# Optimization experiments

Measured on AMD Instinct MI355X. Metric: run time of the kernel, lower is better.

The kernel has to match this reference:

```python
import jax, jax.numpy as jnp
import numpy as np

N_NODES = 100000


def _gcn_conv(x, W, b, src, dst, num_nodes):
    """PyG GCNConv: h = x @ W; symmetric-normalized scatter-add over edges
    (self-loops already included in src/dst); out = aggregate + b."""
    h = x @ W  # [N, out]
    ones = jnp.ones(src.shape[0], dtype=x.dtype)
    deg = jax.ops.segment_sum(ones, dst, num_segments=num_nodes)  # in-degree incl self-loop
    dinv = jnp.where(deg > 0, jax.lax.rsqrt(deg), 0.0)
    norm = dinv[src] * dinv[dst]  # [E]
    msg = h[src] * norm[:, None]  # [E, out] -- dominant memory traffic
    out = jax.ops.segment_sum(msg, dst, num_segments=num_nodes)
    return out + b


def setup_inputs() -> dict:
    key = jax.random.key(0)
    k = jax.random.split(key, 4)
    in_c, hid, out_c = 128, 64, 32
    n_edges = 1600000
    x = jax.random.normal(k[0], (N_NODES, in_c), dtype=jnp.float32)
    edge_index = jax.random.randint(k[1], (2, n_edges), 0, N_NODES, dtype=jnp.int64)
    W1 = jax.random.normal(k[2], (in_c, hid), dtype=jnp.float32) * (1.0 / np.sqrt(in_c))
    b1 = jnp.zeros((hid,), dtype=jnp.float32)
    W2 = jax.random.normal(k[3], (hid, out_c), dtype=jnp.float32) * (1.0 / np.sqrt(hid))
    b2 = jnp.zeros((out_c,), dtype=jnp.float32)
    return {"x": x, "edge_index": edge_index, "W1": W1, "b1": b1, "W2": W2, "b2": b2}


def reference(x, edge_index, W1, b1, W2, b2):
    num_nodes = x.shape[0]
    loops = jnp.arange(num_nodes, dtype=edge_index.dtype)
    src = jnp.concatenate([edge_index[0], loops])  # add self-loops once, shared by both layers
    dst = jnp.concatenate([edge_index[1], loops])
    h = _gcn_conv(x, W1, b1, src, dst, num_nodes)
    h = jax.nn.relu(h)
    out = _gcn_conv(h, W2, b2, src, dst, num_nodes)
    return out
```

## Files before the change

kernel.cpp:

```cpp
#include <hip/hip_runtime.h>


#define NBKT(n) (((n) + 127) >> 7)

__device__ inline float bf2f(unsigned short u) {
    union { unsigned int i; float f; } v;
    v.i = ((unsigned int)u) << 16;
    return v.f;
}
__device__ inline unsigned short f2bf(float f) {
    union { float f; unsigned int i; } v;
    v.f = f;
    unsigned int u = v.i;
    return (unsigned short)((u + 0x7fff + ((u >> 16) & 1)) >> 16);
}

#define BH_CHUNK 4096
__global__ void __launch_bounds__(256) bhist_kernel(
        const int* __restrict__ dst, int E, int nbk, int* __restrict__ bcnt) {
    __shared__ int cnt[NBKT(100000)];
    const int t = threadIdx.x;
    const int beg = blockIdx.x * BH_CHUNK;
    const int end = min(E, beg + BH_CHUNK);
    for (int b = t; b < nbk; b += 256) cnt[b] = 0;
    __syncthreads();
    for (int i = beg + t; i < end; i += 256) atomicAdd(&cnt[dst[i] >> 7], 1);
    __syncthreads();
    for (int b = t; b < nbk; b += 256) {
        int c = cnt[b];
        if (c) atomicAdd(&bcnt[b], c);
    }
}

__global__ void bscan_kernel(const int* __restrict__ bcnt, int nbk, int E,
                             int* __restrict__ boffs, int* __restrict__ gcursor) {
    __shared__ int s[1024];
    const int t = threadIdx.x;
    int v = (t < nbk) ? bcnt[t] : 0;
    s[t] = v;
    __syncthreads();
    for (int off = 1; off < 1024; off <<= 1) {
        int x = (t >= off) ? s[t - off] : 0;
        __syncthreads();
        s[t] += x;
        __syncthreads();
    }
    if (t < nbk) {
        int excl = s[t] - v;
        boffs[t] = excl;
        gcursor[t] = excl;
    }
    if (t == 0) boffs[nbk] = E;
}

#define BF_CHUNK 4096
__global__ void __launch_bounds__(256) binfill_kernel(
        const int* __restrict__ src, const int* __restrict__ dst, int E, int nbk,
        int* __restrict__ gcursor, int* __restrict__ entries) {
    __shared__ int cnt[NBKT(100000)];
    __shared__ int gbase[NBKT(100000)];
    __shared__ int rank[NBKT(100000)];
    const int t = threadIdx.x;
    const int beg = blockIdx.x * BF_CHUNK;
    const int end = min(E, beg + BF_CHUNK);
    for (int b = t; b < nbk; b += 256) cnt[b] = 0;
    __syncthreads();
    for (int i = beg + t; i < end; i += 256) atomicAdd(&cnt[dst[i] >> 7], 1);
    __syncthreads();
    for (int b = t; b < nbk; b += 256) {
        int c = cnt[b];
        gbase[b] = c ? atomicAdd(&gcursor[b], c) : 0;
        rank[b] = 0;
    }
    __syncthreads();
    for (int i = beg + t; i < end; i += 256) {
        int d = dst[i];
        int b = d >> 7;
        int r = atomicAdd(&rank[b], 1);
        entries[gbase[b] + r] = (src[i] << 7) | (d & 127);
    }
}

#define FMA4(ACC, AV, WV) \
    ACC.x += (AV) * (WV).x; ACC.y += (AV) * (WV).y; ACC.z += (AV) * (WV).z; ACC.w += (AV) * (WV).w;

__device__ __forceinline__ void gemm1_body(
        const float* __restrict__ A, const float* __restrict__ W,
        unsigned short* __restrict__ out, int N, int row0, float* Wl) {
    constexpr int K = 128, C = 64, F4R = 32, CG = 16;
    const int t = threadIdx.x;
    for (int i = t; i < K * C / 4; i += 256) ((float4*)Wl)[i] = ((const float4*)W)[i];
    __syncthreads();

    const int c0 = (t % CG) * 4;
    const int r0 = (t / CG) * 4;
    const int r_0 = min(row0 + r0 + 0, N - 1);
    const int r_1 = min(row0 + r0 + 1, N - 1);
    const int r_2 = min(row0 + r0 + 2, N - 1);
    const int r_3 = min(row0 + r0 + 3, N - 1);
    const float4* A4 = (const float4*)A;

    float4 acc0 = {0, 0, 0, 0}, acc1 = {0, 0, 0, 0}, acc2 = {0, 0, 0, 0}, acc3 = {0, 0, 0, 0};

#pragma unroll 2
    for (int k4 = 0; k4 < F4R; ++k4) {
        float4 a0 = A4[(size_t)r_0 * F4R + k4];
        float4 a1 = A4[(size_t)r_1 * F4R + k4];
        float4 a2 = A4[(size_t)r_2 * F4R + k4];
        float4 a3 = A4[(size_t)r_3 * F4R + k4];
        float4 w0 = *(const float4*)(Wl + (k4 * 4 + 0) * C + c0);
        float4 w1 = *(const float4*)(Wl + (k4 * 4 + 1) * C + c0);
        float4 w2 = *(const float4*)(Wl + (k4 * 4 + 2) * C + c0);
        float4 w3 = *(const float4*)(Wl + (k4 * 4 + 3) * C + c0);
        FMA4(acc0, a0.x, w0) FMA4(acc1, a1.x, w0) FMA4(acc2, a2.x, w0) FMA4(acc3, a3.x, w0)
        FMA4(acc0, a0.y, w1) FMA4(acc1, a1.y, w1) FMA4(acc2, a2.y, w1) FMA4(acc3, a3.y, w1)
        FMA4(acc0, a0.z, w2) FMA4(acc1, a1.z, w2) FMA4(acc2, a2.z, w2) FMA4(acc3, a3.z, w2)
        FMA4(acc0, a0.w, w3) FMA4(acc1, a1.w, w3) FMA4(acc2, a2.w, w3) FMA4(acc3, a3.w, w3)
    }

    const int row = row0 + r0;
#pragma unroll
    for (int i = 0; i < 4; ++i) {
        int rr = row + i;
        if (rr < N) {
            float4 fr = (i == 0) ? acc0 : (i == 1) ? acc1 : (i == 2) ? acc2 : acc3;
            ushort4 o;
            o.x = f2bf(fr.x); o.y = f2bf(fr.y); o.z = f2bf(fr.z); o.w = f2bf(fr.w);
            *(ushort4*)(out + (size_t)rr * C + c0) = o;
        }
    }
}

__global__ void __launch_bounds__(256) fusedB_kernel(
        const int* __restrict__ entries, const int* __restrict__ boffs, int nbk,
        int* __restrict__ offs, int* __restrict__ csr_src, float* __restrict__ dinv,
        int N, int E,
        const float* __restrict__ x, const float* __restrict__ W1,
        unsigned short* __restrict__ h1u) {
    __shared__ float smem[8192];
    if ((int)blockIdx.x < nbk) {
        int* cnt = (int*)smem;
        int* s = cnt + 128;
        int* rank = s + 128;
        const int t = threadIdx.x;
        const int b = blockIdx.x;
        const int beg = boffs[b];
        const int end = boffs[b + 1];
        if (t < 128) { cnt[t] = 0; rank[t] = 0; }
        __syncthreads();
        for (int i = beg + t; i < end; i += 256) atomicAdd(&cnt[entries[i] & 127], 1);
        __syncthreads();
        if (t < 128) s[t] = cnt[t];
        __syncthreads();
        for (int off = 1; off < 128; off <<= 1) {
            int x2 = 0;
            if (t < 128 && t >= off) x2 = s[t - off];
            __syncthreads();
            if (t < 128) s[t] += x2;
            __syncthreads();
        }
        const int node0 = b * 128;
        if (t < 128 && node0 + t < N) {
            offs[node0 + t] = beg + s[t] - cnt[t];
            dinv[node0 + t] = rsqrtf((float)cnt[t] + 1.0f);
        }
        if (b == 0 && t == 0) offs[N] = E;
        __syncthreads();
        for (int i = beg + t; i < end; i += 256) {
            int e = entries[i];
            int d = e & 127;
            int r = atomicAdd(&rank[d], 1);
            csr_src[beg + s[d] - cnt[d] + r] = (int)((unsigned)e >> 7);
        }
    } else {
        int row0 = (blockIdx.x - nbk) * 64;
        gemm1_body(x, W1, h1u, N, row0, smem);
    }
}

__global__ void __launch_bounds__(256) scale_h1_kernel(
        unsigned short* __restrict__ h, const float* __restrict__ dinv, int N) {
    int idx = blockIdx.x * 256 + threadIdx.x;
    if (idx >= N * 8) return;
    float d = dinv[idx >> 3];
    uint4* p = (uint4*)h + idx;
    uint4 v = *p;
#define SCH(U) { \
        float lo = bf2f((unsigned short)((U) & 0xffffu)) * d; \
        float hi = bf2f((unsigned short)((U) >> 16)) * d; \
        (U) = (unsigned)f2bf(lo) | ((unsigned)f2bf(hi) << 16); }
    SCH(v.x) SCH(v.y) SCH(v.z) SCH(v.w)
#undef SCH
    *p = v;
}

template <int K, int C, int BR>
__global__ void __launch_bounds__(256) gemm2_kernel(
        const unsigned short* __restrict__ A, const float* __restrict__ W,
        const float* __restrict__ dinv, unsigned short* __restrict__ out, int N) {
    constexpr int F4R = K / 4;
    constexpr int CG = C / 4;
    static_assert(256 / CG * 4 == BR, "geometry");
    __shared__ float Wl[K * C];
    __shared__ float Al[BR * K];

    const int t = threadIdx.x;
    for (int i = t; i < K * C / 4; i += 256) ((float4*)Wl)[i] = ((const float4*)W)[i];
    const int row0 = blockIdx.x * BR;
    for (int i = t; i < BR * F4R; i += 256) {
        int r = i / F4R, k4 = i % F4R;
        float4 v = make_float4(0.f, 0.f, 0.f, 0.f);
        if (row0 + r < N) {
            ushort4 u = ((const ushort4*)A)[(size_t)(row0 + r) * F4R + k4];
            v.x = bf2f(u.x); v.y = bf2f(u.y); v.z = bf2f(u.z); v.w = bf2f(u.w);
        }
        *(float4*)(Al + r * K + k4 * 4) = v;
    }
    __syncthreads();

    const int c0 = (t % CG) * 4;
    const int r0 = (t / CG) * 4;
    const float* Ab = Al + r0 * K;
    float4 acc0 = {0, 0, 0, 0}, acc1 = {0, 0, 0, 0}, acc2 = {0, 0, 0, 0}, acc3 = {0, 0, 0, 0};

#pragma unroll 2
    for (int k4 = 0; k4 < K / 4; ++k4) {
        float4 a0 = *(const float4*)(Ab + 0 * K + k4 * 4);
        float4 a1 = *(const float4*)(Ab + 1 * K + k4 * 4);
        float4 a2 = *(const float4*)(Ab + 2 * K + k4 * 4);
        float4 a3 = *(const float4*)(Ab + 3 * K + k4 * 4);
        float4 w0 = *(const float4*)(Wl + (k4 * 4 + 0) * C + c0);
        float4 w1 = *(const float4*)(Wl + (k4 * 4 + 1) * C + c0);
        float4 w2 = *(const float4*)(Wl + (k4 * 4 + 2) * C + c0);
        float4 w3 = *(const float4*)(Wl + (k4 * 4 + 3) * C + c0);
        FMA4(acc0, a0.x, w0) FMA4(acc1, a1.x, w0) FMA4(acc2, a2.x, w0) FMA4(acc3, a3.x, w0)
        FMA4(acc0, a0.y, w1) FMA4(acc1, a1.y, w1) FMA4(acc2, a2.y, w1) FMA4(acc3, a3.y, w1)
        FMA4(acc0, a0.z, w2) FMA4(acc1, a1.z, w2) FMA4(acc2, a2.z, w2) FMA4(acc3, a3.z, w2)
        FMA4(acc0, a0.w, w3) FMA4(acc1, a1.w, w3) FMA4(acc2, a2.w, w3) FMA4(acc3, a3.w, w3)
    }

    const int row = row0 + r0;
#pragma unroll
    for (int i = 0; i < 4; ++i) {
        int rr = row + i;
        if (rr < N) {
            float d = dinv[rr];
            float4 fr = (i == 0) ? acc0 : (i == 1) ? acc1 : (i == 2) ? acc2 : acc3;
            ushort4 o;
            o.x = f2bf(fr.x * d); o.y = f2bf(fr.y * d);
            o.z = f2bf(fr.z * d); o.w = f2bf(fr.w * d);
            *(ushort4*)(out + (size_t)rr * C + c0) = o;
        }
    }
}

#define G64_LOAD(SS) bf2f(hs[(size_t)(SS) * 64 + lane])
__global__ void __launch_bounds__(256) gather64_kernel(
        const unsigned short* __restrict__ hs, const float* __restrict__ dinv,
        const int* __restrict__ offs, const int* __restrict__ csr_src,
        const float* __restrict__ b, unsigned short* __restrict__ out, int N) {
    const int lane = threadIdx.x & 63;
    const int d = blockIdx.x * 4 + (threadIdx.x >> 6);
    if (d >= N) return;
    const int beg = offs[d];
    const int end = offs[d + 1];
    float acc0 = G64_LOAD(d);
    float acc1 = 0.f, acc2 = 0.f, acc3 = 0.f;
    int j = beg;
    for (; j + 15 < end; j += 16) {
        int s0 = csr_src[j + 0], s1 = csr_src[j + 1], s2 = csr_src[j + 2], s3 = csr_src[j + 3];
        int s4 = csr_src[j + 4], s5 = csr_src[j + 5], s6 = csr_src[j + 6], s7 = csr_src[j + 7];
        int s8 = csr_src[j + 8], s9 = csr_src[j + 9], sa = csr_src[j + 10], sb = csr_src[j + 11];
        int sc = csr_src[j + 12], sd = csr_src[j + 13], se = csr_src[j + 14], sf = csr_src[j + 15];
        float v0 = G64_LOAD(s0), v1 = G64_LOAD(s1), v2 = G64_LOAD(s2), v3 = G64_LOAD(s3);
        float v4 = G64_LOAD(s4), v5 = G64_LOAD(s5), v6 = G64_LOAD(s6), v7 = G64_LOAD(s7);
        float v8 = G64_LOAD(s8), v9 = G64_LOAD(s9), va = G64_LOAD(sa), vb = G64_LOAD(sb);
        float vc = G64_LOAD(sc), vd = G64_LOAD(sd), ve = G64_LOAD(se), vf = G64_LOAD(sf);
        acc0 += v0; acc1 += v1; acc2 += v2; acc3 += v3;
        acc0 += v4; acc1 += v5; acc2 += v6; acc3 += v7;
        acc0 += v8; acc1 += v9; acc2 += va; acc3 += vb;
        acc0 += vc; acc1 += vd; acc2 += ve; acc3 += vf;
    }
    if (j + 7 < end) {
        int s0 = csr_src[j + 0], s1 = csr_src[j + 1], s2 = csr_src[j + 2], s3 = csr_src[j + 3];
        int s4 = csr_src[j + 4], s5 = csr_src[j + 5], s6 = csr_src[j + 6], s7 = csr_src[j + 7];
        float v0 = G64_LOAD(s0), v1 = G64_LOAD(s1), v2 = G64_LOAD(s2), v3 = G64_LOAD(s3);
        float v4 = G64_LOAD(s4), v5 = G64_LOAD(s5), v6 = G64_LOAD(s6), v7 = G64_LOAD(s7);
        acc0 += v0; acc1 += v1; acc2 += v2; acc3 += v3;
        acc0 += v4; acc1 += v5; acc2 += v6; acc3 += v7;
        j += 8;
    }
    if (j + 3 < end) {
        int s0 = csr_src[j + 0], s1 = csr_src[j + 1], s2 = csr_src[j + 2], s3 = csr_src[j + 3];
        acc0 += G64_LOAD(s0); acc1 += G64_LOAD(s1); acc2 += G64_LOAD(s2); acc3 += G64_LOAD(s3);
        j += 4;
    }
    for (; j < end; ++j) acc0 += G64_LOAD(csr_src[j]);
    float r = ((acc0 + acc1) + (acc2 + acc3)) * dinv[d] + b[lane];
    r = fmaxf(r, 0.f);
    out[(size_t)d * 64 + lane] = f2bf(r);
}

#define G32_LOAD(SS) bf2f(hs[(size_t)(SS) * 32 + lane])
__global__ void __launch_bounds__(256) gather32_kernel(
        const unsigned short* __restrict__ hs, const float* __restrict__ dinv,
        const int* __restrict__ offs, const int* __restrict__ csr_src,
        const float* __restrict__ b, float* __restrict__ out, int N) {
    const int lane = threadIdx.x & 31;
    const int d = blockIdx.x * 8 + (threadIdx.x >> 5);
    if (d >= N) return;
    const int beg = offs[d];
    const int end = offs[d + 1];
    float acc0 = G32_LOAD(d);
    float acc1 = 0.f, acc2 = 0.f, acc3 = 0.f;
    int j = beg;
    for (; j + 15 < end; j += 16) {
        int s0 = csr_src[j + 0], s1 = csr_src[j + 1], s2 = csr_src[j + 2], s3 = csr_src[j + 3];
        int s4 = csr_src[j + 4], s5 = csr_src[j + 5], s6 = csr_src[j + 6], s7 = csr_src[j + 7];
        int s8 = csr_src[j + 8], s9 = csr_src[j + 9], sa = csr_src[j + 10], sb = csr_src[j + 11];
        int sc = csr_src[j + 12], sd = csr_src[j + 13], se = csr_src[j + 14], sf = csr_src[j + 15];
        float v0 = G32_LOAD(s0), v1 = G32_LOAD(s1), v2 = G32_LOAD(s2), v3 = G32_LOAD(s3);
        float v4 = G32_LOAD(s4), v5 = G32_LOAD(s5), v6 = G32_LOAD(s6), v7 = G32_LOAD(s7);
        float v8 = G32_LOAD(s8), v9 = G32_LOAD(s9), va = G32_LOAD(sa), vb = G32_LOAD(sb);
        float vc = G32_LOAD(sc), vd = G32_LOAD(sd), ve = G32_LOAD(se), vf = G32_LOAD(sf);
        acc0 += v0; acc1 += v1; acc2 += v2; acc3 += v3;
        acc0 += v4; acc1 += v5; acc2 += v6; acc3 += v7;
        acc0 += v8; acc1 += v9; acc2 += va; acc3 += vb;
        acc0 += vc; acc1 += vd; acc2 += ve; acc3 += vf;
    }
    if (j + 7 < end) {
        int s0 = csr_src[j + 0], s1 = csr_src[j + 1], s2 = csr_src[j + 2], s3 = csr_src[j + 3];
        int s4 = csr_src[j + 4], s5 = csr_src[j + 5], s6 = csr_src[j + 6], s7 = csr_src[j + 7];
        float v0 = G32_LOAD(s0), v1 = G32_LOAD(s1), v2 = G32_LOAD(s2), v3 = G32_LOAD(s3);
        float v4 = G32_LOAD(s4), v5 = G32_LOAD(s5), v6 = G32_LOAD(s6), v7 = G32_LOAD(s7);
        acc0 += v0; acc1 += v1; acc2 += v2; acc3 += v3;
        acc0 += v4; acc1 += v5; acc2 += v6; acc3 += v7;
        j += 8;
    }
    if (j + 3 < end) {
        int s0 = csr_src[j + 0], s1 = csr_src[j + 1], s2 = csr_src[j + 2], s3 = csr_src[j + 3];
        acc0 += G32_LOAD(s0); acc1 += G32_LOAD(s1); acc2 += G32_LOAD(s2); acc3 += G32_LOAD(s3);
        j += 4;
    }
    for (; j < end; ++j) acc0 += G32_LOAD(csr_src[j]);
    float r = ((acc0 + acc1) + (acc2 + acc3)) * dinv[d] + b[lane];
    out[(size_t)d * 32 + lane] = r;
}

extern "C" void kernel_launch(void* const* d_in, const int* in_sizes, int n_in,
                              void* d_out, int out_size, void* d_ws, size_t ws_size,
                              hipStream_t stream) {
    const float* x = (const float*)d_in[0];
    const int* ei = (const int*)d_in[1];
    const float* W1 = (const float*)d_in[2];
    const float* b1 = (const float*)d_in[3];
    const float* W2 = (const float*)d_in[4];
    const float* b2 = (const float*)d_in[5];

    const int N = in_sizes[0] / 128;
    const int E = in_sizes[1] / 2;
    const int* src = ei;
    const int* dst = ei + E;
    const int nbk = NBKT(N);

    int* bcnt = (int*)d_ws;
    int* boffs = bcnt + 1024;
    int* gcursor = boffs + 1024;
    float* dinv = (float*)(gcursor + 1024);
    int* offs = (int*)(dinv + ((N + 255) & ~255));
    int* entries = offs + ((N + 1 + 255) & ~255);
    int* csr_src = entries + ((E + 255) & ~255);
    unsigned short* h1u = (unsigned short*)(csr_src + ((E + 255) & ~255));
    unsigned short* h2b = h1u + (size_t)N * 64;
    unsigned short* h3s = h1u;
    float* out = (float*)d_out;

    const int GB = (N + 63) / 64;

    hipMemsetAsync(bcnt, 0, 1024 * 4, stream);
    bhist_kernel<<<(E + BH_CHUNK - 1) / BH_CHUNK, 256, 0, stream>>>(dst, E, nbk, bcnt);
    bscan_kernel<<<1, 1024, 0, stream>>>(bcnt, nbk, E, boffs, gcursor);

    binfill_kernel<<<(E + BF_CHUNK - 1) / BF_CHUNK, 256, 0, stream>>>(src, dst, E, nbk, gcursor, entries);

    fusedB_kernel<<<nbk + GB, 256, 0, stream>>>(entries, boffs, nbk, offs, csr_src, dinv,
                                                N, E, x, W1, h1u);

    scale_h1_kernel<<<(N * 8 + 255) / 256, 256, 0, stream>>>(h1u, dinv, N);

    gather64_kernel<<<(N + 3) / 4, 256, 0, stream>>>(h1u, dinv, offs, csr_src, b1, h2b, N);

    gemm2_kernel<64, 32, 128><<<(N + 127) / 128, 256, 0, stream>>>(h2b, W2, dinv, h3s, N);

    gather32_kernel<<<(N + 7) / 8, 256, 0, stream>>>(h3s, dinv, offs, csr_src, b2, out, N);
}
```

Baseline: 199.5 us.

## Split fused CSR/GEMM1 kernel and fold dinv scaling into GEMM1 epilogue

Splits the combined bucket-to-CSR and GEMM1 kernel into two kernels run in sequence, so GEMM1 can read dinv and scale its output rows before the bf16 conversion. This drops the separate scale_h1 pass, which re-read and re-wrote the whole N×64 bf16 buffer. The cost is that the CSR build and GEMM1 no longer overlap inside one launch, and there is one extra kernel boundary between them. The bucket kernel also now uses only small static shared memory instead of a 32 KB array.

```diff
diff --git a/kernel.cpp b/kernel.cpp
--- a/kernel.cpp
+++ b/kernel.cpp
@@ -81,17 +81,58 @@
     }
 }
 
+__global__ void __launch_bounds__(256) bucket2csr_kernel(
+        const int* __restrict__ entries, const int* __restrict__ boffs, int nbk,
+        int* __restrict__ offs, int* __restrict__ csr_src, float* __restrict__ dinv,
+        int N, int E) {
+    __shared__ int cnt[128];
+    __shared__ int s[128];
+    __shared__ int rank[128];
+    const int t = threadIdx.x;
+    const int b = blockIdx.x;
+    const int beg = boffs[b];
+    const int end = boffs[b + 1];
+    if (t < 128) { cnt[t] = 0; rank[t] = 0; }
+    __syncthreads();
+    for (int i = beg + t; i < end; i += 256) atomicAdd(&cnt[entries[i] & 127], 1);
+    __syncthreads();
+    if (t < 128) s[t] = cnt[t];
+    __syncthreads();
+    for (int off = 1; off < 128; off <<= 1) {
+        int x = 0;
+        if (t < 128 && t >= off) x = s[t - off];
+        __syncthreads();
+        if (t < 128) s[t] += x;
+        __syncthreads();
+    }
+    const int node0 = b * 128;
+    if (t < 128 && node0 + t < N) {
+        offs[node0 + t] = beg + s[t] - cnt[t];
+        dinv[node0 + t] = rsqrtf((float)cnt[t] + 1.0f);
+    }
+    if (b == 0 && t == 0) offs[N] = E;
+    __syncthreads();
+    for (int i = beg + t; i < end; i += 256) {
+        int e = entries[i];
+        int d = e & 127;
+        int r = atomicAdd(&rank[d], 1);
+        csr_src[beg + s[d] - cnt[d] + r] = (int)((unsigned)e >> 7);
+    }
+}
+
 #define FMA4(ACC, AV, WV) \
     ACC.x += (AV) * (WV).x; ACC.y += (AV) * (WV).y; ACC.z += (AV) * (WV).z; ACC.w += (AV) * (WV).w;
 
-__device__ __forceinline__ void gemm1_body(
+__global__ void __launch_bounds__(256) gemm1_kernel(
         const float* __restrict__ A, const float* __restrict__ W,
-        unsigned short* __restrict__ out, int N, int row0, float* Wl) {
+        const float* __restrict__ dinv, unsigned short* __restrict__ out, int N) {
     constexpr int K = 128, C = 64, F4R = 32, CG = 16;
+    __shared__ float Wl[K * C];
     const int t = threadIdx.x;
     for (int i = t; i < K * C / 4; i += 256) ((float4*)Wl)[i] = ((const float4*)W)[i];
     __syncthreads();
 
+    const int row0 = blockIdx.x * 64;
     const int c0 = (t % CG) * 4;
     const int r0 = (t / CG) * 4;
     const int r_0 = min(row0 + r0 + 0, N - 1);
@@ -123,75 +164,14 @@
     for (int i = 0; i < 4; ++i) {
         int rr = row + i;
         if (rr < N) {
+            float d = dinv[rr];
             float4 fr = (i == 0) ? acc0 : (i == 1) ? acc1 : (i == 2) ? acc2 : acc3;
             ushort4 o;
-            o.x = f2bf(fr.x); o.y = f2bf(fr.y); o.z = f2bf(fr.z); o.w = f2bf(fr.w);
+            o.x = f2bf(fr.x * d); o.y = f2bf(fr.y * d);
+            o.z = f2bf(fr.z * d); o.w = f2bf(fr.w * d);
             *(ushort4*)(out + (size_t)rr * C + c0) = o;
         }
     }
-}
-
-__global__ void __launch_bounds__(256) fusedB_kernel(
-        const int* __restrict__ entries, const int* __restrict__ boffs, int nbk,
-        int* __restrict__ offs, int* __restrict__ csr_src, float* __restrict__ dinv,
-        int N, int E,
-        const float* __restrict__ x, const float* __restrict__ W1,
-        unsigned short* __restrict__ h1u) {
-    __shared__ float smem[8192];
-    if ((int)blockIdx.x < nbk) {
-        int* cnt = (int*)smem;
-        int* s = cnt + 128;
-        int* rank = s + 128;
-        const int t = threadIdx.x;
-        const int b = blockIdx.x;
-        const int beg = boffs[b];
-        const int end = boffs[b + 1];
-        if (t < 128) { cnt[t] = 0; rank[t] = 0; }
-        __syncthreads();
-        for (int i = beg + t; i < end; i += 256) atomicAdd(&cnt[entries[i] & 127], 1);
-        __syncthreads();
-        if (t < 128) s[t] = cnt[t];
-        __syncthreads();
-        for (int off = 1; off < 128; off <<= 1) {
-            int x2 = 0;
-            if (t < 128 && t >= off) x2 = s[t - off];
-            __syncthreads();
-            if (t < 128) s[t] += x2;
-            __syncthreads();
-        }
-        const int node0 = b * 128;
-        if (t < 128 && node0 + t < N) {
-            offs[node0 + t] = beg + s[t] - cnt[t];
-            dinv[node0 + t] = rsqrtf((float)cnt[t] + 1.0f);
-        }
-        if (b == 0 && t == 0) offs[N] = E;
-        __syncthreads();
-        for (int i = beg + t; i < end; i += 256) {
-            int e = entries[i];
-            int d = e & 127;
-            int r = atomicAdd(&rank[d], 1);
-            csr_src[beg + s[d] - cnt[d] + r] = (int)((unsigned)e >> 7);
-        }
-    } else {
-        int row0 = (blockIdx.x - nbk) * 64;
-        gemm1_body(x, W1, h1u, N, row0, smem);
-    }
-}
-
-__global__ void __launch_bounds__(256) scale_h1_kernel(
-        unsigned short* __restrict__ h, const float* __restrict__ dinv, int N) {
-    int idx = blockIdx.x * 256 + threadIdx.x;
-    if (idx >= N * 8) return;
-    float d = dinv[idx >> 3];
-    uint4* p = (uint4*)h + idx;
-    uint4 v = *p;
-#define SCH(U) { \
-        float lo = bf2f((unsigned short)((U) & 0xffffu)) * d; \
-        float hi = bf2f((unsigned short)((U) >> 16)) * d; \
-        (U) = (unsigned)f2bf(lo) | ((unsigned)f2bf(hi) << 16); }
-    SCH(v.x) SCH(v.y) SCH(v.z) SCH(v.w)
-#undef SCH
-    *p = v;
 }
 
 template <int K, int C, int BR>
@@ -370,12 +350,10 @@
     int* offs = (int*)(dinv + ((N + 255) & ~255));
     int* entries = offs + ((N + 1 + 255) & ~255);
     int* csr_src = entries + ((E + 255) & ~255);
-    unsigned short* h1u = (unsigned short*)(csr_src + ((E + 255) & ~255));
-    unsigned short* h2b = h1u + (size_t)N * 64;
-    unsigned short* h3s = h1u;
+    unsigned short* h1s = (unsigned short*)(csr_src + ((E + 255) & ~255));
+    unsigned short* h2b = h1s + (size_t)N * 64;
+    unsigned short* h3s = h1s;
     float* out = (float*)d_out;
-
-    const int GB = (N + 63) / 64;
 
     hipMemsetAsync(bcnt, 0, 1024 * 4, stream);
     bhist_kernel<<<(E + BH_CHUNK - 1) / BH_CHUNK, 256, 0, stream>>>(dst, E, nbk, bcnt);
@@ -383,12 +361,11 @@
 
     binfill_kernel<<<(E + BF_CHUNK - 1) / BF_CHUNK, 256, 0, stream>>>(src, dst, E, nbk, gcursor, entries);
 
-    fusedB_kernel<<<nbk + GB, 256, 0, stream>>>(entries, boffs, nbk, offs, csr_src, dinv,
-                                                N, E, x, W1, h1u);
-
-    scale_h1_kernel<<<(N * 8 + 255) / 256, 256, 0, stream>>>(h1u, dinv, N);
-
-    gather64_kernel<<<(N + 3) / 4, 256, 0, stream>>>(h1u, dinv, offs, csr_src, b1, h2b, N);
+    bucket2csr_kernel<<<nbk, 256, 0, stream>>>(entries, boffs, nbk, offs, csr_src, dinv, N, E);
+
+    gemm1_kernel<<<(N + 63) / 64, 256, 0, stream>>>(x, W1, dinv, h1s, N);
+
+    gather64_kernel<<<(N + 3) / 4, 256, 0, stream>>>(h1s, dinv, offs, csr_src, b1, h2b, N);
 
     gemm2_kernel<64, 32, 128><<<(N + 127) / 128, 256, 0, stream>>>(h2b, W2, dinv, h3s, N);
 
```

New measurement: 198.8 us. No clear change (-0.3%).
